# Optimization experiments

Measured on AMD Instinct MI355X. Metric: run time of the kernel, lower is better.

Reference implementation:

```python
import jax, jax.numpy as jnp
import numpy as np

B, S, D, H = 2, 2048, 1024, 16
HD = D // H  # 64

def setup_inputs() -> dict:
    key = jax.random.key(0)
    ks = jax.random.split(key, 8)
    scale = 0.02
    return {
        "hidden_states": jax.random.normal(ks[0], (B, S, D), jnp.float32),
        "attention_mask": jnp.zeros((B, 1, 1, S), jnp.float32),
        "bias_matrix_chunk": jax.random.normal(ks[1], (S, S), jnp.float32),
        "bias_coef": jax.random.uniform(ks[2], (1,), jnp.float32),
        "Wq": jax.random.normal(ks[3], (D, D), jnp.float32) * scale,
        "bq": jnp.zeros((D,), jnp.float32),
        "Wk": jax.random.normal(ks[4], (D, D), jnp.float32) * scale,
        "bk": jnp.zeros((D,), jnp.float32),
        "Wv": jax.random.normal(ks[5], (D, D), jnp.float32) * scale,
        "bv": jnp.zeros((D,), jnp.float32),
    }

def reference(hidden_states, attention_mask, bias_matrix_chunk, bias_coef,
              Wq, bq, Wk, bk, Wv, bv):
    # q/k/v projections: [B,S,D] -> [B,H,S,HD]
    def heads(x):
        return x.reshape(B, S, H, HD).transpose(0, 2, 1, 3)
    q = heads(hidden_states @ Wq + bq)
    k = heads(hidden_states @ Wk + bk)
    v = heads(hidden_states @ Wv + bv)
    scores = jnp.einsum("bhqd,bhkd->bhqk", q, k) / jnp.sqrt(jnp.float32(HD))
    # custom additive bias, broadcast over batch and heads
    scores = scores + bias_matrix_chunk[None, None, :, :] * bias_coef[0]
    scores = scores + attention_mask  # additive mask [B,1,1,S]
    probs = jax.nn.softmax(scores, axis=-1)  # dropout prob 0 -> identity
    ctx = jnp.einsum("bhqk,bhkd->bhqd", probs, v)
    return ctx.transpose(0, 2, 1, 3).reshape(B, S, D)
```

## Files before the change

kernel.cpp:

```cpp
#include <hip/hip_runtime.h>

typedef unsigned short u16;
typedef __attribute__((ext_vector_type(8))) short bf16x8;
typedef __attribute__((ext_vector_type(4))) float f32x4;
typedef __attribute__((ext_vector_type(8))) unsigned short u16x8;
typedef __attribute__((ext_vector_type(4))) unsigned short u16x4;
typedef __attribute__((ext_vector_type(4))) float f32x4v;

#define LOG2E 1.4426950408889634f
#define QSCALE 0.18033688011112042f

#define SB 2048
#define DB 1024
#define NH 16
#define HD 64

__device__ __forceinline__ u16 f2bf(float f) {
  unsigned u = __float_as_uint(f);
  return (u16)((u + 0x7FFFu + ((u >> 16) & 1u)) >> 16);
}
__device__ __forceinline__ float bf2f(u16 h) {
  return __uint_as_float(((unsigned)h) << 16);
}
__device__ __forceinline__ unsigned cvt_pk_bf16(float lo, float hi) {
  unsigned r;
  asm("v_cvt_pk_bf16_f32 %0, %1, %2" : "=v"(r) : "v"(lo), "v"(hi));
  return r;
}

__device__ __forceinline__ void gload_lds16(const void* g, void* l) {
  __builtin_amdgcn_global_load_lds((const __attribute__((address_space(1))) void*)g,
                                   (__attribute__((address_space(3))) void*)l, 16, 0, 0);
}


__global__ void conv_x_kernel(const float* __restrict__ in, u16* __restrict__ out) {
  int i = blockIdx.x * blockDim.x + threadIdx.x;
  const f32x4v* p = (const f32x4v*)in + (size_t)i * 2;
  f32x4v a = p[0], b = p[1];
  u16x8 o;
  o[0] = f2bf(a[0]); o[1] = f2bf(a[1]); o[2] = f2bf(a[2]); o[3] = f2bf(a[3]);
  o[4] = f2bf(b[0]); o[5] = f2bf(b[1]); o[6] = f2bf(b[2]); o[7] = f2bf(b[3]);
  *((u16x8*)out + i) = o;
}

__global__ void conv_wt_kernel(const float* __restrict__ Wq, const float* __restrict__ Wk,
                               const float* __restrict__ Wv, u16* __restrict__ Wt) {
  __shared__ float tile[32][33];
  int z = blockIdx.z;
  const float* W = (z == 0) ? Wq : (z == 1) ? Wk : Wv;
  int k0 = blockIdx.x * 32, n0 = blockIdx.y * 32;
  int tx = threadIdx.x;
  for (int i = threadIdx.y; i < 32; i += 8)
    tile[i][tx] = W[(size_t)(k0 + i) * DB + n0 + tx];
  __syncthreads();
  for (int i = threadIdx.y; i < 32; i += 8)
    Wt[(size_t)z * DB * DB + (size_t)(n0 + i) * DB + k0 + tx] = f2bf(tile[tx][i]);
}

__global__ __launch_bounds__(256) void conv_biasr_kernel(
    const float* __restrict__ biasM, const float* __restrict__ coef,
    const float* __restrict__ mask, u16* __restrict__ biasR) {
  __shared__ float tile[64 * 64];
  __shared__ float msh[64];
  int ktb = blockIdx.x, q64b = blockIdx.y, b = blockIdx.z;
  int q0 = q64b * 64, k0 = ktb * 64;
  int tid = threadIdx.x;
  float c = coef[0] * LOG2E;
  for (int i = tid; i < 4096; i += 256)
    tile[i] = biasM[(size_t)(q0 + (i >> 6)) * SB + k0 + (i & 63)];
  if (tid < 64) msh[tid] = mask[b * SB + k0 + tid] * LOG2E;
  __syncthreads();
  int wid = tid >> 6, lane = tid & 63, lrow = lane & 15, lk = lane >> 4;
  int qloc = wid * 16 + lrow;
  u16x8 o0, o1;
#pragma unroll
  for (int e = 0; e < 16; e++) {
    int kloc = (e >> 2) * 16 + lk * 4 + (e & 3);
    float v = tile[qloc * 64 + kloc] * c + msh[kloc];
    if (e < 8) o0[e] = f2bf(v); else o1[e - 8] = f2bf(v);
  }
  int widp = (q64b & 1) * 4 + wid;
  size_t base = ((((size_t)b * 16 + (q64b >> 1)) * 32 + ktb) * 8 + widp) * 1024 + lane * 16;
  *(u16x8*)&biasR[base] = o0;
  *(u16x8*)&biasR[base + 8] = o1;
}

__global__ __launch_bounds__(256) void gemm_qkv_kernel(
    const u16* __restrict__ X, const u16* __restrict__ Wt,
    const float* __restrict__ bq, const float* __restrict__ bk, const float* __restrict__ bv,
    u16* __restrict__ Q, u16* __restrict__ K, u16* __restrict__ V) {
  __shared__ __align__(16) u16 As[128 * 32];
  __shared__ __align__(16) u16 Bs[128 * 32];
  int z = blockIdx.z;
  const u16* Wz = Wt + (size_t)z * DB * DB;
  const float* bias = (z == 0) ? bq : (z == 1) ? bk : bv;
  int m0 = blockIdx.x * 128, n0 = blockIdx.y * 128;
  int tid = threadIdx.x, wid = tid >> 6, lane = tid & 63;
  int wr = wid >> 1, wc = wid & 1;
  int lrow = lane & 15, lk = lane >> 4;
  int srow = lane >> 2, scol = (lane & 3) * 8;

  f32x4 acc[4][4];
#pragma unroll
  for (int i = 0; i < 4; i++)
#pragma unroll
    for (int j = 0; j < 4; j++) acc[i][j] = (f32x4){0.f, 0.f, 0.f, 0.f};

  for (int k0 = 0; k0 < DB; k0 += 32) {
#pragma unroll
    for (int p = 0; p < 2; p++) {
      int c = p * 4 + wid;
      gload_lds16(X + (size_t)(m0 + c * 16 + srow) * DB + k0 + scol, &As[c * 512]);
      gload_lds16(Wz + (size_t)(n0 + c * 16 + srow) * DB + k0 + scol, &Bs[c * 512]);
    }
    __syncthreads();
    bf16x8 af[4], bf_[4];
#pragma unroll
    for (int i = 0; i < 4; i++)
      af[i] = *(const bf16x8*)&As[(wr * 64 + i * 16 + lrow) * 32 + lk * 8];
#pragma unroll
    for (int j = 0; j < 4; j++)
      bf_[j] = *(const bf16x8*)&Bs[(wc * 64 + j * 16 + lrow) * 32 + lk * 8];
#pragma unroll
    for (int i = 0; i < 4; i++)
#pragma unroll
      for (int j = 0; j < 4; j++)
        acc[i][j] = __builtin_amdgcn_mfma_f32_16x16x32_bf16(af[i], bf_[j], acc[i][j], 0, 0, 0);
    __syncthreads();
  }

#pragma unroll
  for (int j = 0; j < 4; j++) {
    int n = n0 + wc * 64 + j * 16 + lrow;
    float bb = bias[n];
    int h = n >> 6, hd = n & 63;
#pragma unroll
    for (int i = 0; i < 4; i++) {
      int mbase = m0 + wr * 64 + i * 16 + lk * 4;
      int b = mbase >> 11;
      int s = mbase & (SB - 1);
      int bh = b * NH + h;
      if (z == 2) {
        u16x4 pk;
#pragma unroll
        for (int r = 0; r < 4; r++) pk[r] = f2bf(acc[i][j][r] + bb);
        size_t idx = ((size_t)bh * HD + hd) * SB + (s & ~63) + (((s & 63)) ^ ((hd & 7) << 3));
        *(u16x4*)&V[idx] = pk;
      } else if (z == 1) {
#pragma unroll
        for (int r = 0; r < 4; r++) {
          int sr = s + r;
          K[((size_t)bh * SB + sr) * HD + (hd ^ ((sr & 7) << 3))] = f2bf(acc[i][j][r] + bb);
        }
      } else {
#pragma unroll
        for (int r = 0; r < 4; r++)
          Q[((size_t)bh * SB + (s + r)) * HD + hd] = f2bf((acc[i][j][r] + bb) * QSCALE);
      }
    }
  }
}

__global__ __launch_bounds__(512) void attn_kernel(
    const u16* __restrict__ Q, const u16* __restrict__ K, const u16* __restrict__ Vt,
    const u16* __restrict__ biasR, float* __restrict__ out) {
  __shared__ __align__(16) u16 Klds[2][4096];
  __shared__ __align__(16) u16 Vlds[2][4096];
  __shared__ __align__(16) u16 P[8][1024];
  __shared__ float Lsh[8][16];
  int h = blockIdx.x;
  int b = blockIdx.y >> 4, q0b = blockIdx.y & 15;
  int bh = b * NH + h;
  int q0 = q0b * 128;
  int tid = threadIdx.x, wid = tid >> 6, lane = tid & 63;
  int lrow = lane & 15, lk = lane >> 4;
  const u16* Qb = Q + (size_t)bh * SB * HD;
  const u16* Kb = K + (size_t)bh * SB * HD;
  const u16* Vb = Vt + (size_t)bh * HD * SB;
  const u16* biasW = biasR + ((((size_t)b * 16 + q0b) * 32) * 8 + wid) * 1024 + lane * 16;

  int qr = q0 + wid * 16 + lrow;
  bf16x8 qf0 = *(const bf16x8*)&Qb[(size_t)qr * HD + lk * 8];
  bf16x8 qf1 = *(const bf16x8*)&Qb[(size_t)qr * HD + 32 + lk * 8];

  int kst = wid * 512 + lane * 8;
  int vrow_st = wid * 8 + (lane >> 3), vslot = lane & 7;

  float l_acc = 0.f;
  f32x4 acc[4];
#pragma unroll
  for (int d = 0; d < 4; d++) acc[d] = (f32x4){0.f, 0.f, 0.f, 0.f};
  u16* Pw = &P[wid][0];

  gload_lds16(Kb + kst, &Klds[0][wid * 512]);
  gload_lds16(Vb + (size_t)vrow_st * SB + vslot * 8, &Vlds[0][wid * 512]);
  u16x8 bc0 = *(const u16x8*)biasW;
  u16x8 bc1 = *(const u16x8*)(biasW + 8);
  __syncthreads();

  for (int ktb = 0; ktb < 32; ktb++) {
    int cur = ktb & 1;
    if (ktb < 31) {
      int ktn = (ktb + 1) * 64;
      gload_lds16(Kb + (size_t)ktn * HD + kst, &Klds[cur ^ 1][wid * 512]);
      gload_lds16(Vb + (size_t)vrow_st * SB + ktn + vslot * 8, &Vlds[cur ^ 1][wid * 512]);
    }
    int ktp = (ktb + 1) & 31;
    u16x8 bn0 = *(const u16x8*)(biasW + (size_t)ktp * 8192);
    u16x8 bn1 = *(const u16x8*)(biasW + (size_t)ktp * 8192 + 8);

    f32x4 s[4];
#pragma unroll
    for (int kb = 0; kb < 4; kb++) {
      int krow = kb * 16 + lrow;
      int sw = (krow & 7) << 3;
      bf16x8 ka0 = *(const bf16x8*)&Klds[cur][krow * 64 + ((lk * 8) ^ sw)];
      bf16x8 ka1 = *(const bf16x8*)&Klds[cur][krow * 64 + ((32 + lk * 8) ^ sw)];
      f32x4 t = __builtin_amdgcn_mfma_f32_16x16x32_bf16(ka0, qf0, (f32x4){0.f, 0.f, 0.f, 0.f}, 0, 0, 0);
      s[kb] = __builtin_amdgcn_mfma_f32_16x16x32_bf16(ka1, qf1, t, 0, 0, 0);
    }
#pragma unroll
    for (int kb = 0; kb < 4; kb++) {
      float pv[4];
#pragma unroll
      for (int r = 0; r < 4; r++) {
        int e = kb * 4 + r;
        float bb = bf2f(e < 8 ? bc0[e] : bc1[e - 8]);
        pv[r] = exp2f(s[kb][r] + bb);
        l_acc += pv[r];
      }
      unsigned d0 = cvt_pk_bf16(pv[0], pv[1]);
      unsigned d1 = cvt_pk_bf16(pv[2], pv[3]);
      int byte = (lrow * 128 + kb * 32 + lk * 8) ^ ((lrow & 7) << 4);
      *(uint2*)((char*)Pw + byte) = make_uint2(d0, d1);
    }
    bc0 = bn0; bc1 = bn1;
    asm volatile("s_waitcnt lgkmcnt(0)" ::: "memory");
    bf16x8 pa[2];
#pragma unroll
    for (int ks = 0; ks < 2; ks++) {
      int byte = (lrow * 128 + ks * 64 + lk * 16) ^ ((lrow & 7) << 4);
      pa[ks] = *(const bf16x8*)((char*)Pw + byte);
    }
#pragma unroll
    for (int db = 0; db < 4; db++) {
      int vrow = db * 16 + lrow;
      int sw = (vrow & 7) << 3;
#pragma unroll
      for (int ks = 0; ks < 2; ks++) {
        bf16x8 vb = *(const bf16x8*)&Vlds[cur][vrow * 64 + ((ks * 32 + lk * 8) ^ sw)];
        acc[db] = __builtin_amdgcn_mfma_f32_16x16x32_bf16(pa[ks], vb, acc[db], 0, 0, 0);
      }
    }
    __syncthreads();
  }
  l_acc += __shfl_xor(l_acc, 16);
  l_acc += __shfl_xor(l_acc, 32);
  if (lk == 0) Lsh[wid][lrow] = l_acc;
  asm volatile("s_waitcnt lgkmcnt(0)" ::: "memory");
  f32x4v lv = *(const f32x4v*)&Lsh[wid][lk * 4];
#pragma unroll
  for (int db = 0; db < 4; db++) {
#pragma unroll
    for (int r = 0; r < 4; r++) {
      int qg = q0 + wid * 16 + lk * 4 + r;
      out[((size_t)b * SB + qg) * DB + h * HD + db * 16 + lrow] = acc[db][r] / lv[r];
    }
  }
}

extern "C" void kernel_launch(void* const* d_in, const int* in_sizes, int n_in,
                              void* d_out, int out_size, void* d_ws, size_t ws_size,
                              hipStream_t stream) {
  const float* hs    = (const float*)d_in[0];
  const float* mask  = (const float*)d_in[1];
  const float* biasM = (const float*)d_in[2];
  const float* coef  = (const float*)d_in[3];
  const float* Wq    = (const float*)d_in[4];
  const float* bq    = (const float*)d_in[5];
  const float* Wk    = (const float*)d_in[6];
  const float* bk    = (const float*)d_in[7];
  const float* Wv    = (const float*)d_in[8];
  const float* bv    = (const float*)d_in[9];
  float* out = (float*)d_out;

  char* w = (char*)d_ws;
  u16* Qb    = (u16*)(w);
  u16* Kb    = (u16*)(w + 8u * 1024 * 1024);
  u16* Vb    = (u16*)(w + 16u * 1024 * 1024);
  u16* X     = (u16*)(w + 24u * 1024 * 1024);
  u16* Wt    = (u16*)(w + 32u * 1024 * 1024);
  u16* biasR = (u16*)(w + 24u * 1024 * 1024);

  conv_x_kernel<<<2048, 256, 0, stream>>>(hs, X);
  conv_wt_kernel<<<dim3(32, 32, 3), dim3(32, 8), 0, stream>>>(Wq, Wk, Wv, Wt);
  gemm_qkv_kernel<<<dim3(32, 8, 3), 256, 0, stream>>>(X, Wt, bq, bk, bv, Qb, Kb, Vb);
  conv_biasr_kernel<<<dim3(32, 32, 2), 256, 0, stream>>>(biasM, coef, mask, biasR);
  attn_kernel<<<dim3(NH, 32), 512, 0, stream>>>(Qb, Kb, Vb, biasR, out);
}
```

Baseline: 232.9 us.

## Fold bias into MFMA accumulator, compute row sums via MFMA, vectorize QK stores

The attention kernel now seeds the QK MFMA accumulator with the bias instead of zero, which removes the separate per-element bias add. It also computes the softmax denominator with an extra MFMA against a vector of ones, replacing the scalar accumulation, the shuffles and the LDS reduction. It adds s_setprio around the MFMA sections and unrolls the key loop by two. The QKV GEMM is split into a Q/K kernel with swapped MFMA operands, so each lane can write four contiguous head-dim values as one vector store, and a separate V kernel. The ones-MFMA adds matrix work and uses the bf16-rounded probabilities for the denominator, and the split GEMM costs one extra launch.

```diff
diff --git a/kernel.cpp b/kernel.cpp
--- a/kernel.cpp
+++ b/kernel.cpp
@@ -86,15 +86,16 @@
   *(u16x8*)&biasR[base + 8] = o1;
 }
 
-__global__ __launch_bounds__(256) void gemm_qkv_kernel(
+__global__ __launch_bounds__(256) void gemm_qk_kernel(
     const u16* __restrict__ X, const u16* __restrict__ Wt,
-    const float* __restrict__ bq, const float* __restrict__ bk, const float* __restrict__ bv,
-    u16* __restrict__ Q, u16* __restrict__ K, u16* __restrict__ V) {
+    const float* __restrict__ bq, const float* __restrict__ bk,
+    u16* __restrict__ Q, u16* __restrict__ K) {
   __shared__ __align__(16) u16 As[128 * 32];
   __shared__ __align__(16) u16 Bs[128 * 32];
   int z = blockIdx.z;
   const u16* Wz = Wt + (size_t)z * DB * DB;
-  const float* bias = (z == 0) ? bq : (z == 1) ? bk : bv;
+  const float* bias = (z == 0) ? bq : bk;
+  u16* dst = (z == 0) ? Q : K;
   int m0 = blockIdx.x * 128, n0 = blockIdx.y * 128;
   int tid = threadIdx.x, wid = tid >> 6, lane = tid & 63;
   int wr = wid >> 1, wc = wid & 1;
@@ -126,6 +127,72 @@
     for (int i = 0; i < 4; i++)
 #pragma unroll
       for (int j = 0; j < 4; j++)
+        acc[i][j] = __builtin_amdgcn_mfma_f32_16x16x32_bf16(bf_[j], af[i], acc[i][j], 0, 0, 0);
+    __syncthreads();
+  }
+
+  int h = (n0 >> 6) + wc;
+#pragma unroll
+  for (int j = 0; j < 4; j++) {
+    int nb = wc * 64 + j * 16 + lk * 4;
+    f32x4v bb4 = *(const f32x4v*)&bias[n0 + nb];
+    int hd0 = nb & 63;
+#pragma unroll
+    for (int i = 0; i < 4; i++) {
+      int m = m0 + wr * 64 + i * 16 + lrow;
+      int b = m >> 11, s = m & (SB - 1);
+      int bh = b * NH + h;
+      u16x4 pk;
+      if (z == 0) {
+#pragma unroll
+        for (int r = 0; r < 4; r++) pk[r] = f2bf((acc[i][j][r] + bb4[r]) * QSCALE);
+        *(u16x4*)&dst[((size_t)bh * SB + s) * HD + hd0] = pk;
+      } else {
+#pragma unroll
+        for (int r = 0; r < 4; r++) pk[r] = f2bf(acc[i][j][r] + bb4[r]);
+        *(u16x4*)&dst[((size_t)bh * SB + s) * HD + (hd0 ^ ((s & 7) << 3))] = pk;
+      }
+    }
+  }
+}
+
+__global__ __launch_bounds__(256) void gemm_v_kernel(
+    const u16* __restrict__ X, const u16* __restrict__ Wt,
+    const float* __restrict__ bv, u16* __restrict__ V) {
+  __shared__ __align__(16) u16 As[128 * 32];
+  __shared__ __align__(16) u16 Bs[128 * 32];
+  const u16* Wz = Wt + (size_t)2 * DB * DB;
+  int m0 = blockIdx.x * 128, n0 = blockIdx.y * 128;
+  int tid = threadIdx.x, wid = tid >> 6, lane = tid & 63;
+  int wr = wid >> 1, wc = wid & 1;
+  int lrow = lane & 15, lk = lane >> 4;
+  int srow = lane >> 2, scol = (lane & 3) * 8;
+
+  f32x4 acc[4][4];
+#pragma unroll
+  for (int i = 0; i < 4; i++)
+#pragma unroll
+    for (int j = 0; j < 4; j++) acc[i][j] = (f32x4){0.f, 0.f, 0.f, 0.f};
+
+  for (int k0 = 0; k0 < DB; k0 += 32) {
+#pragma unroll
+    for (int p = 0; p < 2; p++) {
+      int c = p * 4 + wid;
+      gload_lds16(X + (size_t)(m0 + c * 16 + srow) * DB + k0 + scol, &As[c * 512]);
+      gload_lds16(Wz + (size_t)(n0 + c * 16 + srow) * DB + k0 + scol, &Bs[c * 512]);
+    }
+    __syncthreads();
+    bf16x8 af[4], bf_[4];
+#pragma unroll
+    for (int i = 0; i < 4; i++)
+      af[i] = *(const bf16x8*)&As[(wr * 64 + i * 16 + lrow) * 32 + lk * 8];
+#pragma unroll
+    for (int j = 0; j < 4; j++)
+      bf_[j] = *(const bf16x8*)&Bs[(wc * 64 + j * 16 + lrow) * 32 + lk * 8];
+#pragma unroll
+    for (int i = 0; i < 4; i++)
+#pragma unroll
+      for (int j = 0; j < 4; j++)
         acc[i][j] = __builtin_amdgcn_mfma_f32_16x16x32_bf16(af[i], bf_[j], acc[i][j], 0, 0, 0);
     __syncthreads();
   }
@@ -133,7 +200,7 @@
 #pragma unroll
   for (int j = 0; j < 4; j++) {
     int n = n0 + wc * 64 + j * 16 + lrow;
-    float bb = bias[n];
+    float bb = bv[n];
     int h = n >> 6, hd = n & 63;
 #pragma unroll
     for (int i = 0; i < 4; i++) {
@@ -141,23 +208,11 @@
       int b = mbase >> 11;
       int s = mbase & (SB - 1);
       int bh = b * NH + h;
-      if (z == 2) {
-        u16x4 pk;
-#pragma unroll
-        for (int r = 0; r < 4; r++) pk[r] = f2bf(acc[i][j][r] + bb);
-        size_t idx = ((size_t)bh * HD + hd) * SB + (s & ~63) + (((s & 63)) ^ ((hd & 7) << 3));
-        *(u16x4*)&V[idx] = pk;
-      } else if (z == 1) {
-#pragma unroll
-        for (int r = 0; r < 4; r++) {
-          int sr = s + r;
-          K[((size_t)bh * SB + sr) * HD + (hd ^ ((sr & 7) << 3))] = f2bf(acc[i][j][r] + bb);
-        }
-      } else {
-#pragma unroll
-        for (int r = 0; r < 4; r++)
-          Q[((size_t)bh * SB + (s + r)) * HD + hd] = f2bf((acc[i][j][r] + bb) * QSCALE);
-      }
+      u16x4 pk;
+#pragma unroll
+      for (int r = 0; r < 4; r++) pk[r] = f2bf(acc[i][j][r] + bb);
+      size_t idx = ((size_t)bh * HD + hd) * SB + (s & ~63) + ((s & 63) ^ ((hd & 7) << 3));
+      *(u16x4*)&V[idx] = pk;
     }
   }
 }
@@ -168,7 +223,6 @@
   __shared__ __align__(16) u16 Klds[2][4096];
   __shared__ __align__(16) u16 Vlds[2][4096];
   __shared__ __align__(16) u16 P[8][1024];
-  __shared__ float Lsh[8][16];
   int h = blockIdx.x;
   int b = blockIdx.y >> 4, q0b = blockIdx.y & 15;
   int bh = b * NH + h;
@@ -184,13 +238,15 @@
   bf16x8 qf0 = *(const bf16x8*)&Qb[(size_t)qr * HD + lk * 8];
   bf16x8 qf1 = *(const bf16x8*)&Qb[(size_t)qr * HD + 32 + lk * 8];
 
+  const bf16x8 vones = {0x3F80, 0x3F80, 0x3F80, 0x3F80, 0x3F80, 0x3F80, 0x3F80, 0x3F80};
+
   int kst = wid * 512 + lane * 8;
   int vrow_st = wid * 8 + (lane >> 3), vslot = lane & 7;
 
-  float l_acc = 0.f;
-  f32x4 acc[4];
+  f32x4 acc[4], accl;
 #pragma unroll
   for (int d = 0; d < 4; d++) acc[d] = (f32x4){0.f, 0.f, 0.f, 0.f};
+  accl = (f32x4){0.f, 0.f, 0.f, 0.f};
   u16* Pw = &P[wid][0];
 
   gload_lds16(Kb + kst, &Klds[0][wid * 512]);
@@ -199,6 +255,7 @@
   u16x8 bc1 = *(const u16x8*)(biasW + 8);
   __syncthreads();
 
+#pragma unroll 2
   for (int ktb = 0; ktb < 32; ktb++) {
     int cur = ktb & 1;
     if (ktb < 31) {
@@ -210,39 +267,49 @@
     u16x8 bn0 = *(const u16x8*)(biasW + (size_t)ktp * 8192);
     u16x8 bn1 = *(const u16x8*)(biasW + (size_t)ktp * 8192 + 8);
 
+    f32x4 bf[4];
+#pragma unroll
+    for (int kb = 0; kb < 4; kb++)
+#pragma unroll
+      for (int r = 0; r < 4; r++) {
+        int e = kb * 4 + r;
+        bf[kb][r] = bf2f(e < 8 ? bc0[e] : bc1[e - 8]);
+      }
+
     f32x4 s[4];
+    __builtin_amdgcn_s_setprio(1);
 #pragma unroll
     for (int kb = 0; kb < 4; kb++) {
       int krow = kb * 16 + lrow;
       int sw = (krow & 7) << 3;
       bf16x8 ka0 = *(const bf16x8*)&Klds[cur][krow * 64 + ((lk * 8) ^ sw)];
       bf16x8 ka1 = *(const bf16x8*)&Klds[cur][krow * 64 + ((32 + lk * 8) ^ sw)];
-      f32x4 t = __builtin_amdgcn_mfma_f32_16x16x32_bf16(ka0, qf0, (f32x4){0.f, 0.f, 0.f, 0.f}, 0, 0, 0);
+      f32x4 t = __builtin_amdgcn_mfma_f32_16x16x32_bf16(ka0, qf0, bf[kb], 0, 0, 0);
       s[kb] = __builtin_amdgcn_mfma_f32_16x16x32_bf16(ka1, qf1, t, 0, 0, 0);
     }
+    __builtin_amdgcn_s_setprio(0);
+
 #pragma unroll
     for (int kb = 0; kb < 4; kb++) {
-      float pv[4];
-#pragma unroll
-      for (int r = 0; r < 4; r++) {
-        int e = kb * 4 + r;
-        float bb = bf2f(e < 8 ? bc0[e] : bc1[e - 8]);
-        pv[r] = exp2f(s[kb][r] + bb);
-        l_acc += pv[r];
-      }
-      unsigned d0 = cvt_pk_bf16(pv[0], pv[1]);
-      unsigned d1 = cvt_pk_bf16(pv[2], pv[3]);
+      float pv0 = exp2f(s[kb][0]), pv1 = exp2f(s[kb][1]);
+      float pv2 = exp2f(s[kb][2]), pv3 = exp2f(s[kb][3]);
+      unsigned d0 = cvt_pk_bf16(pv0, pv1);
+      unsigned d1 = cvt_pk_bf16(pv2, pv3);
       int byte = (lrow * 128 + kb * 32 + lk * 8) ^ ((lrow & 7) << 4);
       *(uint2*)((char*)Pw + byte) = make_uint2(d0, d1);
     }
     bc0 = bn0; bc1 = bn1;
     asm volatile("s_waitcnt lgkmcnt(0)" ::: "memory");
+
     bf16x8 pa[2];
 #pragma unroll
     for (int ks = 0; ks < 2; ks++) {
       int byte = (lrow * 128 + ks * 64 + lk * 16) ^ ((lrow & 7) << 4);
       pa[ks] = *(const bf16x8*)((char*)Pw + byte);
     }
+    __builtin_amdgcn_s_setprio(1);
+    accl = __builtin_amdgcn_mfma_f32_16x16x32_bf16(pa[0], vones, accl, 0, 0, 0);
+    accl = __builtin_amdgcn_mfma_f32_16x16x32_bf16(pa[1], vones, accl, 0, 0, 0);
 #pragma unroll
     for (int db = 0; db < 4; db++) {
       int vrow = db * 16 + lrow;
@@ -253,19 +320,19 @@
         acc[db] = __builtin_amdgcn_mfma_f32_16x16x32_bf16(pa[ks], vb, acc[db], 0, 0, 0);
       }
     }
-    __syncthreads();
-  }
-  l_acc += __shfl_xor(l_acc, 16);
-  l_acc += __shfl_xor(l_acc, 32);
-  if (lk == 0) Lsh[wid][lrow] = l_acc;
-  asm volatile("s_waitcnt lgkmcnt(0)" ::: "memory");
-  f32x4v lv = *(const f32x4v*)&Lsh[wid][lk * 4];
+    __builtin_amdgcn_s_setprio(0);
+    __syncthreads();
+  }
+
+  float inv[4];
+#pragma unroll
+  for (int r = 0; r < 4; r++) inv[r] = 1.0f / accl[r];
 #pragma unroll
   for (int db = 0; db < 4; db++) {
 #pragma unroll
     for (int r = 0; r < 4; r++) {
       int qg = q0 + wid * 16 + lk * 4 + r;
-      out[((size_t)b * SB + qg) * DB + h * HD + db * 16 + lrow] = acc[db][r] / lv[r];
+      out[((size_t)b * SB + qg) * DB + h * HD + db * 16 + lrow] = acc[db][r] * inv[r];
     }
   }
 }
@@ -295,7 +362,8 @@
 
   conv_x_kernel<<<2048, 256, 0, stream>>>(hs, X);
   conv_wt_kernel<<<dim3(32, 32, 3), dim3(32, 8), 0, stream>>>(Wq, Wk, Wv, Wt);
-  gemm_qkv_kernel<<<dim3(32, 8, 3), 256, 0, stream>>>(X, Wt, bq, bk, bv, Qb, Kb, Vb);
+  gemm_qk_kernel<<<dim3(32, 8, 2), 256, 0, stream>>>(X, Wt, bq, bk, Qb, Kb);
+  gemm_v_kernel<<<dim3(32, 8, 1), 256, 0, stream>>>(X, Wt, bv, Vb);
   conv_biasr_kernel<<<dim3(32, 32, 2), 256, 0, stream>>>(biasM, coef, mask, biasR);
   attn_kernel<<<dim3(NH, 32), 512, 0, stream>>>(Qb, Kb, Vb, biasR, out);
 }
```

Result: faster. 227.2 us (-2.5%).
